# Performance work log

Hardware: AMD Instinct MI355X
Metric: run time of the kernel (lower is better)

The kernel has to match this reference:

```python
import jax, jax.numpy as jnp
import numpy as np

B, S, D, H = 2, 2048, 1024, 16
DK = D // H

def setup_inputs() -> dict:
    key = jax.random.key(0)
    ks = jax.random.split(key, 8)
    return {
        "query": jax.random.normal(ks[0], (B, S, D), dtype=jnp.float32),
        "key": jax.random.normal(ks[1], (B, S, D), dtype=jnp.float32),
        "value": jax.random.normal(ks[2], (B, S, D), dtype=jnp.float32),
        "mask": jax.random.randint(ks[3], (B, S, S), 0, 2, dtype=jnp.int32),
        "w_q": jax.random.normal(ks[4], (D, D), dtype=jnp.float32) * (D ** -0.5),
        "w_k": jax.random.normal(ks[5], (D, D), dtype=jnp.float32) * (D ** -0.5),
        "w_v": jax.random.normal(ks[6], (D, D), dtype=jnp.float32) * (D ** -0.5),
        "w_o": jax.random.normal(ks[7], (D, D), dtype=jnp.float32) * (D ** -0.5),
    }

def reference(query, key, value, mask, w_q, w_k, w_v, w_o):
    b, s, d = query.shape
    # Linear projections (torch nn.Linear: x @ W.T); here w_* are [out, in]
    Q = jnp.einsum('bsd,ed->bse', query, w_q).reshape(b, s, H, DK).transpose(0, 2, 1, 3)
    K = jnp.einsum('bsd,ed->bse', key, w_k).reshape(b, s, H, DK).transpose(0, 2, 1, 3)
    V = jnp.einsum('bsd,ed->bse', value, w_v).reshape(b, s, H, DK).transpose(0, 2, 1, 3)
    scale = jnp.float32(DK ** 0.5)
    scores = jnp.einsum('bhqd,bhkd->bhqk', Q, K) / scale  # [B,H,S,S]
    scores = jnp.where(mask[:, None, :, :] == 0, jnp.float32(-1e9), scores)
    attn = jax.nn.softmax(scores, axis=-1)  # dropout p=0 -> identity
    out = jnp.einsum('bhqk,bhkd->bhqd', attn, V)  # [B,H,S,DK]
    out = out.transpose(0, 2, 1, 3).reshape(b, s, d)
    return jnp.einsum('bsd,ed->bse', out, w_o)
```

## Files before the change

kernel.cpp:

```cpp
#include <hip/hip_runtime.h>
#include <stdint.h>

#define B_ 2
#define S_ 2048
#define D_ 1024
#define H_ 16
#define DK_ 64

typedef __attribute__((ext_vector_type(8))) short short8;
typedef __attribute__((ext_vector_type(4))) float f32x4;

__device__ __forceinline__ short f2bf(float f) {
    uint32_t u = __float_as_uint(f);
    return (short)((u + 0x7FFFu + ((u >> 16) & 1u)) >> 16);
}

__device__ __forceinline__ float fexp2(float x) {
    float r;
    asm("v_exp_f32 %0, %1" : "=v"(r) : "v"(x));
    return r;
}

__device__ __forceinline__ uint32_t cvt_pk_bf16(float lo, float hi) {
    uint32_t r;
    asm("v_cvt_pk_bf16_f32 %0, %1, %2" : "=v"(r) : "v"(lo), "v"(hi));
    return r;
}

#define GLOAD16(gptr, lptr)                                                      \
    __builtin_amdgcn_global_load_lds(                                            \
        (const __attribute__((address_space(1))) void*)(gptr),                   \
        (__attribute__((address_space(3))) void*)(lptr), 16, 0, 0)

__global__ __launch_bounds__(256) void cast_qkv(const float* __restrict__ a,
                                                const float* __restrict__ b,
                                                const float* __restrict__ c,
                                                short* __restrict__ oa,
                                                short* __restrict__ ob,
                                                short* __restrict__ oc) {
    int bid = blockIdx.x;
    int sel = bid >> 11;
    int i = (bid & 2047) * 256 + threadIdx.x;
    const float* in = (sel == 0) ? a : (sel == 1) ? b : c;
    short* out = (sel == 0) ? oa : (sel == 1) ? ob : oc;
    const float4* p = ((const float4*)in) + (size_t)i * 2;
    float4 x = p[0], y = p[1];
    short8 o;
    o[0] = f2bf(x.x); o[1] = f2bf(x.y); o[2] = f2bf(x.z); o[3] = f2bf(x.w);
    o[4] = f2bf(y.x); o[5] = f2bf(y.y); o[6] = f2bf(y.z); o[7] = f2bf(y.w);
    *(((short8*)out) + i) = o;
}

__global__ __launch_bounds__(256) void cast_w4(const float* __restrict__ a,
                                               const float* __restrict__ b,
                                               const float* __restrict__ c,
                                               const float* __restrict__ d,
                                               short* __restrict__ oa,
                                               short* __restrict__ ob,
                                               short* __restrict__ oc,
                                               short* __restrict__ od) {
    int bid = blockIdx.x;
    int sel = bid >> 9;
    int i = (bid & 511) * 256 + threadIdx.x;
    const float* in = (sel == 0) ? a : (sel == 1) ? b : (sel == 2) ? c : d;
    short* out = (sel == 0) ? oa : (sel == 1) ? ob : (sel == 2) ? oc : od;
    const float4* p = ((const float4*)in) + (size_t)i * 2;
    float4 x = p[0], y = p[1];
    short8 o;
    o[0] = f2bf(x.x); o[1] = f2bf(x.y); o[2] = f2bf(x.z); o[3] = f2bf(x.w);
    o[4] = f2bf(y.x); o[5] = f2bf(y.y); o[6] = f2bf(y.z); o[7] = f2bf(y.w);
    *(((short8*)out) + i) = o;
}

__global__ __launch_bounds__(256) void pack_mask(const int* __restrict__ mask,
                                                 uint32_t* __restrict__ packed,
                                                 float* __restrict__ lut) {
    if (blockIdx.x == 0 && threadIdx.x < 64) {
        int e = threadIdx.x >> 2, r = threadIdx.x & 3;
        lut[threadIdx.x] = __int_as_float(((e >> r) & 1) ? 0x7F800000u : 0xFF800000u);
    }
    size_t t = (size_t)blockIdx.x * 256 + threadIdx.x;
    int4 m = ((const int4*)mask)[t];
    uint32_t nib = (m.x != 0 ? 1u : 0u) | (m.y != 0 ? 2u : 0u) |
                   (m.z != 0 ? 4u : 0u) | (m.w != 0 ? 8u : 0u);
    int lane = threadIdx.x & 63;
    uint32_t v = nib << ((lane & 7) * 4);
    v |= __shfl_xor(v, 1);
    v |= __shfl_xor(v, 2);
    v |= __shfl_xor(v, 4);
    if ((lane & 7) == 0) packed[t >> 3] = v;
}

#define GEMM_BODY(A, W, C, F32OUT, Mv, Nv, Kv)                                              \
    __shared__ short As[128 * 32];                                                          \
    __shared__ short Bs[128 * 32];                                                          \
    const int tid = threadIdx.x;                                                            \
    const int lane = tid & 63;                                                              \
    const int w = tid >> 6;                                                                 \
    const int wm = w >> 1, wn = w & 1;                                                      \
    const int mBase = blockIdx.y * 128, nBase = blockIdx.x * 128;                           \
    f32x4 acc[4][4];                                                                        \
    _Pragma("unroll") for (int i = 0; i < 4; i++)                                           \
        _Pragma("unroll") for (int j = 0; j < 4; j++) acc[i][j] = (f32x4)0.f;               \
    const int srow = lane >> 2;                                                             \
    const int sslot = lane & 3;                                                             \
    for (int k0 = 0; k0 < Kv; k0 += 32) {                                                   \
        _Pragma("unroll") for (int i = 0; i < 2; ++i) {                                     \
            int seg = w * 2 + i;                                                            \
            int row = seg * 16 + srow;                                                      \
            const short* ga = A + (size_t)(mBase + row) * Kv + k0 + sslot * 8;              \
            GLOAD16(ga, (char*)As + seg * 1024);                                            \
            const short* gb = W + (size_t)(nBase + row) * Kv + k0 + sslot * 8;              \
            GLOAD16(gb, (char*)Bs + seg * 1024);                                            \
        }                                                                                   \
        asm volatile("s_waitcnt vmcnt(0)" ::: "memory");                                    \
        __syncthreads();                                                                    \
        short8 af[4], bfv[4];                                                               \
        _Pragma("unroll") for (int mi = 0; mi < 4; mi++)                                    \
            af[mi] = *(const short8*)&As[(wm * 64 + mi * 16 + (lane & 15)) * 32 + (lane >> 4) * 8]; \
        _Pragma("unroll") for (int ni = 0; ni < 4; ni++)                                    \
            bfv[ni] = *(const short8*)&Bs[(wn * 64 + ni * 16 + (lane & 15)) * 32 + (lane >> 4) * 8]; \
        _Pragma("unroll") for (int mi = 0; mi < 4; mi++)                                    \
            _Pragma("unroll") for (int ni = 0; ni < 4; ni++)                                \
                acc[mi][ni] = __builtin_amdgcn_mfma_f32_16x16x32_bf16(af[mi], bfv[ni], acc[mi][ni], 0, 0, 0); \
        __syncthreads();                                                                    \
    }                                                                                       \
    _Pragma("unroll") for (int mi = 0; mi < 4; mi++)                                        \
        _Pragma("unroll") for (int ni = 0; ni < 4; ni++)                                    \
            _Pragma("unroll") for (int r = 0; r < 4; r++) {                                 \
                int row = mBase + wm * 64 + mi * 16 + (lane >> 4) * 4 + r;                  \
                int col = nBase + wn * 64 + ni * 16 + (lane & 15);                          \
                float v = acc[mi][ni][r];                                                   \
                if (F32OUT) ((float*)C)[(size_t)row * Nv + col] = v;                        \
                else        ((short*)C)[(size_t)row * Nv + col] = f2bf(v);                  \
            }

__global__ __launch_bounds__(256) void gemm3_nt(const short* __restrict__ A0, const short* __restrict__ W0, short* __restrict__ C0,
                                                const short* __restrict__ A1, const short* __restrict__ W1, short* __restrict__ C1,
                                                const short* __restrict__ A2, const short* __restrict__ W2, short* __restrict__ C2) {
    const int z = blockIdx.z;
    const short* A = (z == 0) ? A0 : (z == 1) ? A1 : A2;
    const short* W = (z == 0) ? W0 : (z == 1) ? W1 : W2;
    short* C = (z == 0) ? C0 : (z == 1) ? C1 : C2;
    GEMM_BODY(A, W, C, 0, (B_ * S_), D_, D_)
}

__global__ __launch_bounds__(256) void gemm_out(const short* __restrict__ A,
                                                const short* __restrict__ W,
                                                float* __restrict__ C) {
    GEMM_BODY(A, W, C, 1, (B_ * S_), D_, D_)
}

__global__ __launch_bounds__(256) void transpose_v(const short* __restrict__ Vp,
                                                   short* __restrict__ Vt) {
    __shared__ short t[64 * 72];
    int bid = blockIdx.x;
    int bh = bid >> 5;
    int st = bid & 31;
    int b = bh >> 4, h = bh & 15;
    int sBase = st * 64;
    int tid = threadIdx.x;
#pragma unroll
    for (int i = 0; i < 2; i++) {
        int ci = i * 256 + tid;
        int sr = ci >> 3, sl = ci & 7;
        short8 v = *(const short8*)&Vp[(size_t)(b * S_ + sBase + sr) * D_ + h * 64 + sl * 8];
#pragma unroll
        for (int j = 0; j < 8; j++) t[(sl * 8 + j) * 72 + sr] = v[j];
    }
    __syncthreads();
#pragma unroll
    for (int i = 0; i < 2; i++) {
        int ci = i * 256 + tid;
        int dk = ci >> 3, sl = ci & 7;
        short8 o = *(const short8*)&t[dk * 72 + sl * 8];
        *(short8*)&Vt[(size_t)((b * H_ + h) * 64 + dk) * S_ + sBase + sl * 8] = o;
    }
}

__global__ __launch_bounds__(256) void attn_kernel(const short* __restrict__ Qp,
                                                   const short* __restrict__ Kp,
                                                   const short* __restrict__ Vt,
                                                   const uint32_t* __restrict__ mp,
                                                   const float* __restrict__ lutg,
                                                   short* __restrict__ Op) {
    __shared__ short Ks[2][64 * 64];
    __shared__ short Vs[2][64 * 64];
    __shared__ short Ps[4 * 16 * 64];
    const int qt = blockIdx.x;
    const int bh = blockIdx.y;
    const int b = bh >> 4, h = bh & 15;
    const int qBase = qt * 64;
    const int tid = threadIdx.x, lane = tid & 63, w = tid >> 6;
    const int lg = lane >> 4;
    const int li = lane & 15;
    const float c1 = 0.18033688011112042f;

    const int q = qBase + w * 16 + li;

    short8 qf[2];
#pragma unroll
    for (int ks = 0; ks < 2; ks++)
        qf[ks] = *(const short8*)&Qp[(size_t)(b * S_ + q) * D_ + h * 64 + lg * 8 + ks * 32];

    const int r0 = tid >> 3, sl = tid & 7;
    const int gs = sl ^ (r0 & 7);
    const short* kg0 = Kp + ((size_t)(b * S_) + r0) * D_ + h * 64 + gs * 8;
    const short* kg1 = kg0 + (size_t)32 * D_;
    const short* vg0 = Vt + ((size_t)bh * 64 + r0) * S_ + gs * 8;
    const short* vg1 = vg0 + (size_t)32 * S_;
    const uint32_t* mrow = mp + ((size_t)(b * S_) + q) * 64;
    char* ldsK = (char*)&Ks[0][0];
    char* ldsV = (char*)&Vs[0][0];
    const int woff = w * 1024;

    GLOAD16(kg0, ldsK + woff);
    GLOAD16(kg1, ldsK + 4096 + woff);
    GLOAD16(vg0, ldsV + woff);
    GLOAD16(vg1, ldsV + 4096 + woff);
    uint2 mw = *(const uint2*)mrow;
    asm volatile("s_waitcnt vmcnt(0)" ::: "memory");
    __syncthreads();

    float m_r = -1e30f, l_r = 0.f;
    f32x4 acc[4];
#pragma unroll
    for (int g = 0; g < 4; g++) acc[g] = (f32x4)0.f;

    short* psw = &Ps[w * 1024];
    int cur = 0;

    for (int kt = 0; kt < S_ / 64; ++kt) {
        f32x4 msk[4];
#pragma unroll
        for (int nt = 0; nt < 4; nt++) {
            uint32_t wd = (nt < 2) ? mw.x : mw.y;
            uint32_t nib = (wd >> (((nt & 1) << 4) + (lg << 2))) & 0xFu;
            msk[nt] = *(const f32x4*)&lutg[nib * 4];
        }

        uint2 mwn;
        if (kt < S_ / 64 - 1) {
            const size_t ko = (size_t)((kt + 1) * 64) * D_;
            const int vo = (kt + 1) * 64;
            const int boff = (cur ^ 1) * 8192 + woff;
            GLOAD16(kg0 + ko, ldsK + boff);
            GLOAD16(kg1 + ko, ldsK + boff + 4096);
            GLOAD16(vg0 + vo, ldsV + boff);
            GLOAD16(vg1 + vo, ldsV + boff + 4096);
            mwn = *(const uint2*)&mrow[(kt + 1) * 2];
        }

        f32x4 sc[4];
        __builtin_amdgcn_s_setprio(1);
#pragma unroll
        for (int nt = 0; nt < 4; nt++) {
            f32x4 c = (f32x4)0.f;
#pragma unroll
            for (int ks = 0; ks < 2; ks++) {
                short8 kf = *(const short8*)&Ks[cur][(nt * 16 + li) * 64 + (((lg + ks * 4) ^ (li & 7)) << 3)];
                c = __builtin_amdgcn_mfma_f32_16x16x32_bf16(kf, qf[ks], c, 0, 0, 0);
            }
            sc[nt] = c;
        }
        __builtin_amdgcn_s_setprio(0);

        float tm = fmaxf(fmaxf(fmaxf(sc[0][0], sc[0][1]), fmaxf(sc[0][2], sc[0][3])),
                         fmaxf(fmaxf(sc[1][0], sc[1][1]), fmaxf(sc[1][2], sc[1][3])));
        tm = fmaxf(tm, fmaxf(fmaxf(fmaxf(sc[2][0], sc[2][1]), fmaxf(sc[2][2], sc[2][3])),
                             fmaxf(fmaxf(sc[3][0], sc[3][1]), fmaxf(sc[3][2], sc[3][3]))));
        tm = fmaxf(tm, __shfl_xor(tm, 16));
        tm = fmaxf(tm, __shfl_xor(tm, 32));

        if (__any((tm - m_r) * c1 > 10.0f)) {
            float mn = fmaxf(m_r, tm);
            float alpha = fexp2((m_r - mn) * c1);
            m_r = mn;
            l_r *= alpha;
#pragma unroll
            for (int g = 0; g < 4; g++) acc[g] *= alpha;
        }
        float mc = m_r * c1;

        float ls = 0.f;
#pragma unroll
        for (int nt = 0; nt < 4; nt++) {
            float e0 = fexp2(fminf(__builtin_fmaf(sc[nt][0], c1, -mc), msk[nt][0]));
            float e1 = fexp2(fminf(__builtin_fmaf(sc[nt][1], c1, -mc), msk[nt][1]));
            float e2 = fexp2(fminf(__builtin_fmaf(sc[nt][2], c1, -mc), msk[nt][2]));
            float e3 = fexp2(fminf(__builtin_fmaf(sc[nt][3], c1, -mc), msk[nt][3]));
            ls += (e0 + e1) + (e2 + e3);
            uint32_t p0 = cvt_pk_bf16(e0, e1);
            uint32_t p1 = cvt_pk_bf16(e2, e3);
            *(uint2*)&psw[li * 64 + (((2 * nt + (lg >> 1)) ^ (li & 7)) << 3) + ((lg & 1) << 2)] =
                make_uint2(p0, p1);
        }
        ls += __shfl_xor(ls, 16);
        ls += __shfl_xor(ls, 32);
        l_r += ls;

        __builtin_amdgcn_s_setprio(1);
#pragma unroll
        for (int ks = 0; ks < 2; ks++) {
            short8 pb = *(const short8*)&psw[li * 64 + (((4 * ks + lg) ^ (li & 7)) << 3)];
#pragma unroll
            for (int g = 0; g < 4; g++) {
                short8 vf = *(const short8*)&Vs[cur][(g * 16 + li) * 64 + (((lg + ks * 4) ^ (li & 7)) << 3)];
                acc[g] = __builtin_amdgcn_mfma_f32_16x16x32_bf16(vf, pb, acc[g], 0, 0, 0);
            }
        }
        __builtin_amdgcn_s_setprio(0);

        asm volatile("s_waitcnt vmcnt(0)" ::: "memory");
        __syncthreads();
        cur ^= 1;
        if (kt < S_ / 64 - 1) mw = mwn;
    }

    float inv = 1.f / l_r;
    short* orow = &Op[(size_t)(b * S_ + q) * D_ + h * 64];
#pragma unroll
    for (int g = 0; g < 4; g++) {
        uint2 o;
        o.x = cvt_pk_bf16(acc[g][0] * inv, acc[g][1] * inv);
        o.y = cvt_pk_bf16(acc[g][2] * inv, acc[g][3] * inv);
        *(uint2*)&orow[g * 16 + lg * 4] = o;
    }
}

extern "C" void kernel_launch(void* const* d_in, const int* in_sizes, int n_in,
                              void* d_out, int out_size, void* d_ws, size_t ws_size,
                              hipStream_t stream) {
    const float* q  = (const float*)d_in[0];
    const float* k  = (const float*)d_in[1];
    const float* v  = (const float*)d_in[2];
    const int*   mk = (const int*)d_in[3];
    const float* wq = (const float*)d_in[4];
    const float* wk = (const float*)d_in[5];
    const float* wv = (const float*)d_in[6];
    const float* wo = (const float*)d_in[7];

    const size_t SZ = (size_t)B_ * S_ * D_;
    const size_t DD = (size_t)D_ * D_;
    const size_t NEED = (6 * SZ + 4 * DD) * 2 + (size_t)B_ * S_ * 64 * 4 + 256;
    if (ws_size < NEED) return;

    short* ws  = (short*)d_ws;
    short* qb  = ws;
    short* kb  = qb + SZ;
    short* vb  = kb + SZ;
    short* wqb = vb + SZ;
    short* wkb = wqb + DD;
    short* wvb = wkb + DD;
    short* wob = wvb + DD;
    short* Qp  = wob + DD;
    short* Kp  = Qp + SZ;
    short* Vp  = Kp + SZ;
    uint32_t* mp = (uint32_t*)(Vp + SZ);
    float* lutg = (float*)(mp + (size_t)B_ * S_ * 64);
    short* Vtr = qb;
    short* Opx = kb;

    dim3 blk(256);
    cast_qkv<<<dim3(3 * 2048), blk, 0, stream>>>(q, k, v, qb, kb, vb);
    cast_w4<<<dim3(4 * 512), blk, 0, stream>>>(wq, wk, wv, wo, wqb, wkb, wvb, wob);
    pack_mask<<<dim3((unsigned)((size_t)B_ * S_ * S_ / 4 / 256)), blk, 0, stream>>>(mk, mp, lutg);

    gemm3_nt<<<dim3(D_ / 128, B_ * S_ / 128, 3), blk, 0, stream>>>(
        qb, wqb, Qp, kb, wkb, Kp, vb, wvb, Vp);

    transpose_v<<<dim3(B_ * H_ * (S_ / 64)), blk, 0, stream>>>(Vp, Vtr);

    attn_kernel<<<dim3(S_ / 64, B_ * H_), blk, 0, stream>>>(Qp, Kp, Vtr, mp, lutg, Opx);

    gemm_out<<<dim3(D_ / 128, B_ * S_ / 128), blk, 0, stream>>>(Opx, wob, (float*)d_out);
}
```

Before: 174.2 us.

## Remap blocks for XCD locality and exchange P via lane shuffles instead of LDS

Adds XCD-aware remapping of block indices in the GEMMs and the attention kernel so that blocks sharing the same rows or heads land on the same XCD and reuse its L2. The attention kernel also drops the LDS staging buffer for the probability tile. P fragments are now kept in registers and swapped between lane groups with shuffles, and the V fragment index is permuted to match. This removes an LDS write/read round trip per tile and frees shared memory, at the cost of extra shuffles and selects.

```diff
diff --git a/kernel.cpp b/kernel.cpp
--- a/kernel.cpp
+++ b/kernel.cpp
@@ -98,7 +98,10 @@
     const int lane = tid & 63;                                                              \
     const int w = tid >> 6;                                                                 \
     const int wm = w >> 1, wn = w & 1;                                                      \
-    const int mBase = blockIdx.y * 128, nBase = blockIdx.x * 128;                           \
+    const int l_ = blockIdx.x + (blockIdx.y << 3);                                          \
+    const int xcd_ = l_ & 7, ii_ = l_ >> 3;                                                 \
+    const int mBase = ((xcd_ << 2) + (ii_ >> 3)) * 128;                                     \
+    const int nBase = (ii_ & 7) * 128;                                                      \
     f32x4 acc[4][4];                                                                        \
     _Pragma("unroll") for (int i = 0; i < 4; i++)                                           \
         _Pragma("unroll") for (int j = 0; j < 4; j++) acc[i][j] = (f32x4)0.f;               \
@@ -186,9 +189,9 @@
                                                    short* __restrict__ Op) {
     __shared__ short Ks[2][64 * 64];
     __shared__ short Vs[2][64 * 64];
-    __shared__ short Ps[4 * 16 * 64];
-    const int qt = blockIdx.x;
-    const int bh = blockIdx.y;
+    const int l_ = blockIdx.x + (blockIdx.y << 5);
+    const int bh = ((l_ & 7) << 2) + (l_ >> 8);
+    const int qt = (l_ >> 3) & 31;
     const int b = bh >> 4, h = bh & 15;
     const int qBase = qt * 64;
     const int tid = threadIdx.x, lane = tid & 63, w = tid >> 6;
@@ -227,7 +230,6 @@
 #pragma unroll
     for (int g = 0; g < 4; g++) acc[g] = (f32x4)0.f;
 
-    short* psw = &Ps[w * 1024];
     int cur = 0;
 
     for (int kt = 0; kt < S_ / 64; ++kt) {
@@ -282,6 +284,7 @@
         }
         float mc = m_r * c1;
 
+        uint32_t u[4][2];
         float ls = 0.f;
 #pragma unroll
         for (int nt = 0; nt < 4; nt++) {
@@ -290,10 +293,8 @@
             float e2 = fexp2(fminf(__builtin_fmaf(sc[nt][2], c1, -mc), msk[nt][2]));
             float e3 = fexp2(fminf(__builtin_fmaf(sc[nt][3], c1, -mc), msk[nt][3]));
             ls += (e0 + e1) + (e2 + e3);
-            uint32_t p0 = cvt_pk_bf16(e0, e1);
-            uint32_t p1 = cvt_pk_bf16(e2, e3);
-            *(uint2*)&psw[li * 64 + (((2 * nt + (lg >> 1)) ^ (li & 7)) << 3) + ((lg & 1) << 2)] =
-                make_uint2(p0, p1);
+            u[nt][0] = cvt_pk_bf16(e0, e1);
+            u[nt][1] = cvt_pk_bf16(e2, e3);
         }
         ls += __shfl_xor(ls, 16);
         ls += __shfl_xor(ls, 32);
@@ -302,11 +303,22 @@
         __builtin_amdgcn_s_setprio(1);
 #pragma unroll
         for (int ks = 0; ks < 2; ks++) {
-            short8 pb = *(const short8*)&psw[li * 64 + (((4 * ks + lg) ^ (li & 7)) << 3)];
+            const uint32_t s00 = u[2 * ks][0], s01 = u[2 * ks][1];
+            const uint32_t s10 = u[2 * ks + 1][0], s11 = u[2 * ks + 1][1];
+            uint32_t e0 = (lg & 1) ? s00 : s10;
+            uint32_t e1 = (lg & 1) ? s01 : s11;
+            uint32_t x0 = (uint32_t)__shfl_xor((int)e0, 16);
+            uint32_t x1 = (uint32_t)__shfl_xor((int)e1, 16);
+            union { uint32_t w4[4]; short8 s8; } pu;
+            pu.w4[0] = (lg & 1) ? x0 : s00;
+            pu.w4[1] = (lg & 1) ? x1 : s01;
+            pu.w4[2] = (lg & 1) ? s10 : x0;
+            pu.w4[3] = (lg & 1) ? s11 : x1;
+            const int f = ks * 4 + ((lg & 1) << 1) + (lg >> 1);
 #pragma unroll
             for (int g = 0; g < 4; g++) {
-                short8 vf = *(const short8*)&Vs[cur][(g * 16 + li) * 64 + (((lg + ks * 4) ^ (li & 7)) << 3)];
-                acc[g] = __builtin_amdgcn_mfma_f32_16x16x32_bf16(vf, pb, acc[g], 0, 0, 0);
+                short8 vf = *(const short8*)&Vs[cur][(g * 16 + li) * 64 + ((f ^ (li & 7)) << 3)];
+                acc[g] = __builtin_amdgcn_mfma_f32_16x16x32_bf16(vf, pu.s8, acc[g], 0, 0, 0);
             }
         }
         __builtin_amdgcn_s_setprio(0);
@@ -371,7 +383,7 @@
 
     transpose_v<<<dim3(B_ * H_ * (S_ / 64)), blk, 0, stream>>>(Vp, Vtr);
 
-    attn_kernel<<<dim3(S_ / 64, B_ * H_), blk, 0, stream>>>(Qp, Kp, Vtr, mp, lutg, Opx);
+    attn_kernel<<<dim3(32, 32), blk, 0, stream>>>(Qp, Kp, Vtr, mp, lutg, Opx);
 
     gemm_out<<<dim3(D_ / 128, B_ * S_ / 128), blk, 0, stream>>>(Opx, wob, (float*)d_out);
 }
```

New measurement: 171.7 us. About the same (-1.4%).
